# Optimization experiments

Measured on AMD Instinct MI355X. Metric: run time of the kernel, lower is better.

The kernel has to match this reference:

```python
import jax, jax.numpy as jnp
import numpy as np

HIDDEN = 1024
N_HEADS = 16
HEAD_DIM = HIDDEN // N_HEADS  # 64
B, N = 2, 2048
SCALE = HIDDEN ** (-0.5)  # NOTE: original scales by full hidden_size, not head_dim


def setup_inputs() -> dict:
    key = jax.random.key(0)
    k1, k2 = jax.random.split(key)
    hidden_states = jax.random.normal(k1, (B, N, HIDDEN), dtype=jnp.float32)
    attention_mask = jnp.ones((B, N), dtype=jnp.int32)
    # per-head no-bias Linear(hidden -> 3*head_dim), stacked: [h, hidden, 3*head_dim]
    W_qkv = jax.random.normal(k2, (N_HEADS, HIDDEN, 3 * HEAD_DIM), dtype=jnp.float32) * (HIDDEN ** -0.5)
    return {"hidden_states": hidden_states, "attention_mask": attention_mask, "W_qkv": W_qkv}


def reference(hidden_states, attention_mask, W_qkv):
    # qkv: [b, h, n, 3*d]
    qkv = jnp.einsum('bnD,hDe->bhne', hidden_states, W_qkv)
    q, k, v = jnp.split(qkv, 3, axis=-1)  # each [b, h, n, d]
    scores = jnp.einsum('bhid,bhjd->bhij', q, k) * SCALE
    mask = attention_mask[:, None, None, :] == 0  # [b,1,1,n]
    scores = jnp.where(mask, -jnp.inf, scores)
    attn = jax.nn.softmax(scores, axis=-1)
    out = jnp.einsum('bhij,bhjd->bhid', attn, v)  # [b, h, n, d]
    # rearrange 'b h n d -> b n (h d)'
    return jnp.transpose(out, (0, 2, 1, 3)).reshape(out.shape[0], out.shape[2], -1)
```

## Files before the change

kernel.cpp:

```cpp
#include <hip/hip_runtime.h>
#include <hip/hip_bf16.h>


#define NH   16
#define HD   64
#define SEQ  2048
#define HID  1024
#define E3   192
#define QSCALE 0.04508422017f
#define MBIAS  -43.2808512f

typedef __attribute__((ext_vector_type(8))) short short8;
typedef __attribute__((ext_vector_type(4))) float f32x4;
typedef __attribute__((ext_vector_type(16))) float f32x16;
typedef unsigned short ushort_t;

#define MFMA16(a, b, c) __builtin_amdgcn_mfma_f32_16x16x32_bf16((a), (b), (c), 0, 0, 0)
#define MFMA32(a, b, c) __builtin_amdgcn_mfma_f32_32x32x16_bf16((a), (b), (c), 0, 0, 0)

#if __has_builtin(__builtin_amdgcn_exp2f)
#define EXP2(x) __builtin_amdgcn_exp2f(x)
#else
#define EXP2(x) exp2f(x)
#endif

static __device__ __forceinline__ ushort_t f2bf(float x) {
    unsigned u = __builtin_bit_cast(unsigned, x);
    unsigned r = u + 0x7fff + ((u >> 16) & 1);
    return (ushort_t)(r >> 16);
}

static __device__ __forceinline__ unsigned pack_trunc(float hi, float lo) {
#if __has_builtin(__builtin_amdgcn_perm)
    return __builtin_amdgcn_perm(__builtin_bit_cast(unsigned, hi),
                                 __builtin_bit_cast(unsigned, lo), 0x07060302u);
#else
    return (__builtin_bit_cast(unsigned, hi) & 0xffff0000u) |
           (__builtin_bit_cast(unsigned, lo) >> 16);
#endif
}

static __device__ __forceinline__ void load_lds16(const void* g, void* l) {
    __builtin_amdgcn_global_load_lds(
        (__attribute__((address_space(1))) void*)(g),
        (__attribute__((address_space(3))) void*)(l), 16, 0, 0);
}

__global__ __launch_bounds__(256) void k_cvt_x(const void* __restrict__ Xv,
                                               ushort_t* __restrict__ Xb,
                                               int* __restrict__ flagp) {
    __shared__ int cnt;
    if (threadIdx.x == 0) cnt = 0;
    __syncthreads();
    const unsigned* X32 = (const unsigned*)Xv;
    if (threadIdx.x < 64) {
        unsigned u = X32[(size_t)blockIdx.x * 2048 + threadIdx.x * 32 + 7];
        int bexp = (u >> 7) & 0xFF;
        if (bexp >= 0x68 && bexp <= 0x90) atomicAdd(&cnt, 1);
    }
    __syncthreads();
    const int isf32 = (cnt < 32);
    if (blockIdx.x == 0 && threadIdx.x == 0) *flagp = isf32;

    const size_t base = ((size_t)blockIdx.x * 256 + threadIdx.x) * 16;
    if (isf32) {
        const float* Xf = (const float*)Xv;
        ushort_t tmp[16];
#pragma unroll
        for (int c = 0; c < 4; ++c) {
            float4 v = *(const float4*)(Xf + base + c * 4);
            tmp[c * 4 + 0] = f2bf(v.x); tmp[c * 4 + 1] = f2bf(v.y);
            tmp[c * 4 + 2] = f2bf(v.z); tmp[c * 4 + 3] = f2bf(v.w);
        }
        *(float4*)(Xb + base)     = ((const float4*)tmp)[0];
        *(float4*)(Xb + base + 8) = ((const float4*)tmp)[1];
    } else {
        const ushort_t* Xh = (const ushort_t*)Xv;
        *(float4*)(Xb + base)     = *(const float4*)(Xh + base);
        *(float4*)(Xb + base + 8) = *(const float4*)(Xh + base + 8);
    }
}

__global__ __launch_bounds__(256) void k_cvt_w(const void* __restrict__ Wv,
                                               ushort_t* __restrict__ Wt,
                                               const int* __restrict__ flagp) {
    __shared__ ushort_t tile[64][72];
    const int isf32 = *flagp;
    const int h  = blockIdx.x;
    const int dt = blockIdx.y;
    const int et = blockIdx.z;
    const int D0 = dt * 64, e0 = et * 64;
    const int t  = threadIdx.x;
#pragma unroll
    for (int r = 0; r < 2; ++r) {
        int row = r * 32 + (t >> 3);
        int col = (t & 7) * 8;
        size_t base = ((size_t)(h * HID + D0 + row)) * E3 + e0 + col;
        if (isf32) {
            const float* Wf = (const float*)Wv;
            float4 a = *(const float4*)(Wf + base);
            float4 c = *(const float4*)(Wf + base + 4);
            tile[row][col + 0] = f2bf(a.x); tile[row][col + 1] = f2bf(a.y);
            tile[row][col + 2] = f2bf(a.z); tile[row][col + 3] = f2bf(a.w);
            tile[row][col + 4] = f2bf(c.x); tile[row][col + 5] = f2bf(c.y);
            tile[row][col + 6] = f2bf(c.z); tile[row][col + 7] = f2bf(c.w);
        } else {
            *(float4*)&tile[row][col] = *(const float4*)((const ushort_t*)Wv + base);
        }
    }
    __syncthreads();
#pragma unroll
    for (int r = 0; r < 2; ++r) {
        int erow = r * 32 + (t >> 3);
        int dcol = (t & 7) * 8;
        ushort_t vals[8];
#pragma unroll
        for (int i = 0; i < 8; ++i) vals[i] = tile[dcol + i][erow];
        *(float4*)(Wt + ((size_t)(h * E3 + e0 + erow)) * HID + D0 + dcol) = *(float4*)vals;
    }
}

__global__ __launch_bounds__(256) void k_qkv(const ushort_t* __restrict__ Xb,
                                             const ushort_t* __restrict__ Wt,
                                             ushort_t* __restrict__ Qb,
                                             ushort_t* __restrict__ Kb,
                                             ushort_t* __restrict__ Vtb) {
    __shared__ __align__(16) ushort_t smem[2 * 128 * 64];
    ushort_t* Xl = smem;
    ushort_t* Wl = smem + 128 * 64;

    const int e0 = blockIdx.x * 128;
    const int m0 = blockIdx.y * 128;
    const int b  = m0 >> 11;
    const int n0 = m0 & 2047;
    const int t = threadIdx.x;
    const int w = t >> 6, lane = t & 63, l15 = lane & 15, quad = lane >> 4;
    const int wrow0 = (w & 1) * 64, wcol0 = (w >> 1) * 64;
    const int srow = lane >> 3;
    const int scb  = (lane & 7) ^ srow;

    f32x4 acc[4][4];
#pragma unroll
    for (int i = 0; i < 4; ++i)
#pragma unroll
        for (int j = 0; j < 4; ++j) acc[i][j] = (f32x4){0.f, 0.f, 0.f, 0.f};

    for (int k0 = 0; k0 < HID; k0 += 64) {
        __syncthreads();
#pragma unroll
        for (int cc = 0; cc < 4; ++cc) {
            const int ch  = w * 4 + cc;
            const int row = ch * 8 + srow;
            load_lds16(Xb + (size_t)(m0 + row) * HID + k0 + scb * 8, &Xl[ch * 512]);
            load_lds16(Wt + (size_t)(e0 + row) * HID + k0 + scb * 8, &Wl[ch * 512]);
        }
        __syncthreads();
#pragma unroll
        for (int kh = 0; kh < 2; ++kh) {
            short8 af[4], bfm[4];
#pragma unroll
            for (int i = 0; i < 4; ++i) {
                const int r = wrow0 + i * 16 + l15;
                af[i] = *(const short8*)&Xl[r * 64 + ((kh * 4 + quad) ^ (r & 7)) * 8];
            }
#pragma unroll
            for (int j = 0; j < 4; ++j) {
                const int r = wcol0 + j * 16 + l15;
                bfm[j] = *(const short8*)&Wl[r * 64 + ((kh * 4 + quad) ^ (r & 7)) * 8];
            }
#pragma unroll
            for (int i = 0; i < 4; ++i)
#pragma unroll
                for (int j = 0; j < 4; ++j)
                    acc[i][j] = MFMA16(af[i], bfm[j], acc[i][j]);
        }
    }

    __syncthreads();
#pragma unroll
    for (int p = 0; p < 2; ++p) {
        const int E0  = e0 + p * 64;
        const int hh  = E0 / 192;
        const int r0p = E0 - hh * 192;
        const int own = ((w >> 1) == p);
        if (r0p < 128) {
            if (own) {
                const float sc = (r0p == 0) ? QSCALE : 1.0f;
#pragma unroll
                for (int i = 0; i < 4; ++i)
#pragma unroll
                    for (int j = 0; j < 4; ++j)
#pragma unroll
                        for (int reg = 0; reg < 4; ++reg)
                            smem[(wrow0 + i * 16 + quad * 4 + reg) * 72 + j * 16 + l15] =
                                f2bf(acc[i][j][reg] * sc);
            }
            __syncthreads();
            ushort_t* dstb = (r0p == 0) ? Qb : Kb;
            const int r = t >> 1, part = t & 1;
            size_t dst = ((size_t)(b * NH + hh) * SEQ + n0 + r) * HD + part * 32;
#pragma unroll
            for (int c = 0; c < 4; ++c)
                *(float4*)(dstb + dst + c * 8) = *(const float4*)&smem[r * 72 + part * 32 + c * 8];
        } else {
            if (own) {
#pragma unroll
                for (int i = 0; i < 4; ++i)
#pragma unroll
                    for (int j = 0; j < 4; ++j)
#pragma unroll
                        for (int reg = 0; reg < 4; ++reg)
                            smem[(j * 16 + l15) * 136 + wrow0 + i * 16 + quad * 4 + reg] =
                                f2bf(acc[i][j][reg]);
            }
            __syncthreads();
            const int dr = t >> 2, part = t & 3;
            size_t dst = ((size_t)(b * NH + hh) * HD + dr) * SEQ + n0 + part * 32;
#pragma unroll
            for (int c = 0; c < 4; ++c)
                *(float4*)(Vtb + dst + c * 8) = *(const float4*)&smem[dr * 136 + part * 32 + c * 8];
        }
        if (p == 0) __syncthreads();
    }
}


#define SMPACK(sv, h0v, h1v)                                                  \
    {                                                                         \
        _Pragma("unroll")                                                     \
        for (int g = 0; g < 4; ++g) {                                         \
            float p0 = EXP2(sv[4*g+0]); float p1 = EXP2(sv[4*g+1]);           \
            float p2 = EXP2(sv[4*g+2]); float p3 = EXP2(sv[4*g+3]);           \
            l_r += (p0 + p1) + (p2 + p3);                                     \
            unsigned a0 = pack_trunc(p1, p0), a1 = pack_trunc(p3, p2);        \
            unsigned b0 = a0, b1 = a1;                                        \
            asm volatile("v_permlane32_swap_b32 %0, %1" : "+v"(a0), "+v"(b0));\
            asm volatile("v_permlane32_swap_b32 %0, %1" : "+v"(a1), "+v"(b1));\
            h0v[g*2+0] = a0; h1v[g*2+0] = b0;                                 \
            h0v[g*2+1] = a1; h1v[g*2+1] = b1;                                 \
        }                                                                     \
    }

#define MAKE_PB(dst, h0v, h1v, GB)                                            \
    {                                                                         \
        unsigned w0_ = hi ? h0v[(GB+1)*2+0] : h0v[(GB)*2+0];                  \
        unsigned w1_ = hi ? h0v[(GB+1)*2+1] : h0v[(GB)*2+1];                  \
        unsigned w2_ = hi ? h1v[(GB+1)*2+0] : h1v[(GB)*2+0];                  \
        unsigned w3_ = hi ? h1v[(GB+1)*2+1] : h1v[(GB)*2+1];                  \
        uint4 u_ = {w0_, w1_, w2_, w3_};                                      \
        dst = __builtin_bit_cast(short8, u_);                                 \
    }

__global__ __launch_bounds__(512, 4) void k_attn(const ushort_t* __restrict__ Qb,
                                                 const ushort_t* __restrict__ Kb,
                                                 const ushort_t* __restrict__ Vtb,
                                                 const int* __restrict__ mask,
                                                 void* __restrict__ outv,
                                                 const int* __restrict__ flagp) {
    __shared__ __align__(16) char smem_raw[73728];
    float* biasl = (float*)(smem_raw + 65536);

    const int isf32 = *flagp;
    const int q0 = blockIdx.x * 128;
    const int bh = blockIdx.y;
    const int b  = bh >> 4, h = bh & 15;
    const int t  = threadIdx.x;
    const int w  = t >> 6, lane = t & 63;
    const int wq = w >> 1, jh = w & 1;
    const int c31 = lane & 31, hi = lane >> 5;
    const int srow8 = lane >> 3;
    const int scb   = (lane & 7) ^ srow8;
    const int vrow4 = lane >> 4;
    const int vb15  = lane & 15;
    const int rx7   = c31 & 7;
    const int rx15  = c31 & 15;

    {
        ushort_t* kb = (ushort_t*)(smem_raw);
        ushort_t* vb = (ushort_t*)(smem_raw + 16384);
#pragma unroll
        for (int c = 0; c < 2; ++c) {
            const int krow = w * 16 + c * 8 + srow8;
            load_lds16(Kb + ((size_t)bh * SEQ + krow) * HD + scb * 8,
                       &kb[(w * 2 + c) * 512]);
            const int vrow = w * 8 + c * 4 + vrow4;
            load_lds16(Vtb + ((size_t)bh * HD + vrow) * SEQ + ((vb15 ^ (vrow & 15)) * 8),
                       &vb[(w * 2 + c) * 512]);
        }
    }

    int lm = 0;
    for (int i = t; i < SEQ; i += 512) {
        int mv = mask[b * SEQ + i];
        biasl[i] = mv ? 0.0f : MBIAS;
        lm |= (mv == 0);
    }
    const int qrow = q0 + wq * 32 + c31;
    short8 qB[4];
#pragma unroll
    for (int ds = 0; ds < 4; ++ds)
        qB[ds] = *(const short8*)(Qb + ((size_t)bh * SEQ + qrow) * HD + ds * 16 + hi * 8);

    const int use_bias = __syncthreads_or(lm);

    const f32x16 z16 = {0.f,0.f,0.f,0.f,0.f,0.f,0.f,0.f,0.f,0.f,0.f,0.f,0.f,0.f,0.f,0.f};
    f32x16 oa = z16, ob = z16;
    float l_r = 0.f;

    for (int j0 = 0; j0 < SEQ; j0 += 128) {
        const int idx = (j0 >> 7) & 1;
        asm volatile("s_waitcnt vmcnt(0)" ::: "memory");
        __builtin_amdgcn_s_barrier();
        asm volatile("" ::: "memory");
        if (j0 + 128 < SEQ) {
            ushort_t* kb2 = (ushort_t*)(smem_raw + (idx ^ 1) * 32768);
            ushort_t* vb2 = kb2 + 8192;
#pragma unroll
            for (int c = 0; c < 2; ++c) {
                const int krow = w * 16 + c * 8 + srow8;
                load_lds16(Kb + ((size_t)bh * SEQ + j0 + 128 + krow) * HD + scb * 8,
                           &kb2[(w * 2 + c) * 512]);
                const int vrow = w * 8 + c * 4 + vrow4;
                load_lds16(Vtb + ((size_t)bh * HD + vrow) * SEQ + j0 + 128 + ((vb15 ^ (vrow & 15)) * 8),
                           &vb2[(w * 2 + c) * 512]);
            }
        }
        ushort_t* kb = (ushort_t*)(smem_raw + idx * 32768);
        ushort_t* vb = kb + 8192;

        const int jr0 = jh * 64 + c31;
        const int jr1 = jh * 64 + 32 + c31;
        f32x16 s0, s1;
        __builtin_amdgcn_s_setprio(1);
#pragma unroll
        for (int ds = 0; ds < 4; ++ds) {
            short8 kf0 = *(const short8*)&kb[jr0 * 64 + (((2 * ds + hi) ^ rx7) * 8)];
            short8 kf1 = *(const short8*)&kb[jr1 * 64 + (((2 * ds + hi) ^ rx7) * 8)];
            s0 = MFMA32(kf0, qB[ds], ds ? s0 : z16);
            s1 = MFMA32(kf1, qB[ds], ds ? s1 : z16);
        }
        __builtin_amdgcn_s_setprio(0);
        if (use_bias) {
#pragma unroll
            for (int g = 0; g < 4; ++g) {
                float4 bj0 = *(const float4*)&biasl[j0 + jh * 64 + 8 * g + 4 * hi];
                float4 bj1 = *(const float4*)&biasl[j0 + jh * 64 + 32 + 8 * g + 4 * hi];
                s0[4*g+0] += bj0.x; s0[4*g+1] += bj0.y; s0[4*g+2] += bj0.z; s0[4*g+3] += bj0.w;
                s1[4*g+0] += bj1.x; s1[4*g+1] += bj1.y; s1[4*g+2] += bj1.z; s1[4*g+3] += bj1.w;
            }
        }

        unsigned h0a[8], h1a[8], h0b[8], h1b[8];
        SMPACK(s0, h0a, h1a);
        SMPACK(s1, h0b, h1b);

        __builtin_amdgcn_s_setprio(1);
#pragma unroll
        for (int half = 0; half < 2; ++half) {
#pragma unroll
            for (int c13 = 0; c13 < 2; ++c13) {
                short8 pb;
                if (half == 0) { MAKE_PB(pb, h0a, h1a, 2 * c13); }
                else           { MAKE_PB(pb, h0b, h1b, 2 * c13); }
                const int pblk = (jh * 4 + half * 2 + c13) * 2 + hi;
                short8 va0 = *(const short8*)&vb[(c31)      * 128 + ((pblk ^ rx15) * 8)];
                short8 va1 = *(const short8*)&vb[(32 + c31) * 128 + ((pblk ^ rx15) * 8)];
                oa = MFMA32(va0, pb, oa);
                ob = MFMA32(va1, pb, ob);
            }
        }
        __builtin_amdgcn_s_setprio(0);
    }

    float l_h = l_r + __shfl_xor(l_r, 32);

    __syncthreads();
    float* Obuf = (float*)smem_raw;
    float* Lbuf = (float*)(smem_raw + 65536);
    const int slot = (wq * 64 + lane) * 36;
    if (jh == 1) {
#pragma unroll
        for (int g = 0; g < 4; ++g) {
            *(float4*)&Obuf[slot + g * 4]      = (float4){oa[4*g], oa[4*g+1], oa[4*g+2], oa[4*g+3]};
            *(float4*)&Obuf[slot + 16 + g * 4] = (float4){ob[4*g], ob[4*g+1], ob[4*g+2], ob[4*g+3]};
        }
        Lbuf[wq * 64 + lane] = l_h;
    }
    __syncthreads();
    float rinv = 0.f;
    if (jh == 0) {
        const float l_tot = l_h + Lbuf[wq * 64 + lane];
        rinv = 1.0f / l_tot;
#pragma unroll
        for (int g = 0; g < 4; ++g) {
            float4 pa = *(const float4*)&Obuf[slot + g * 4];
            float4 pb4 = *(const float4*)&Obuf[slot + 16 + g * 4];
            oa[4*g] += pa.x; oa[4*g+1] += pa.y; oa[4*g+2] += pa.z; oa[4*g+3] += pa.w;
            ob[4*g] += pb4.x; ob[4*g+1] += pb4.y; ob[4*g+2] += pb4.z; ob[4*g+3] += pb4.w;
        }
    }
    __syncthreads();

    const int qlr = wq * 32 + c31;
    const int r = t >> 2, part = t & 3;
    if (!isf32) {
        ushort_t* Ol = (ushort_t*)smem_raw;
        if (jh == 0) {
#pragma unroll
            for (int dt = 0; dt < 2; ++dt) {
                const f32x16 ov = dt ? ob : oa;
#pragma unroll
                for (int g = 0; g < 4; ++g) {
                    const int d0 = dt * 32 + 8 * g + 4 * hi;
                    uint2 u;
                    u.x = (unsigned)f2bf(ov[4*g+0] * rinv) | ((unsigned)f2bf(ov[4*g+1] * rinv) << 16);
                    u.y = (unsigned)f2bf(ov[4*g+2] * rinv) | ((unsigned)f2bf(ov[4*g+3] * rinv) << 16);
                    *(uint2*)&Ol[qlr * 72 + d0] = u;
                }
            }
        }
        __syncthreads();
        ushort_t* outp = (ushort_t*)outv;
        size_t dst = ((size_t)b * SEQ + q0 + r) * HID + h * HD + part * 16;
        float4 v0 = *(const float4*)&Ol[r * 72 + part * 16];
        float4 v1 = *(const float4*)&Ol[r * 72 + part * 16 + 8];
        *(float4*)(outp + dst)     = v0;
        *(float4*)(outp + dst + 8) = v1;
    } else {
        float* Olf = (float*)smem_raw;
        if (jh == 0) {
#pragma unroll
            for (int dt = 0; dt < 2; ++dt) {
                const f32x16 ov = dt ? ob : oa;
#pragma unroll
                for (int g = 0; g < 4; ++g) {
                    const int d0 = dt * 32 + 8 * g + 4 * hi;
                    float4 fv;
                    fv.x = ov[4*g+0] * rinv; fv.y = ov[4*g+1] * rinv;
                    fv.z = ov[4*g+2] * rinv; fv.w = ov[4*g+3] * rinv;
                    *(float4*)&Olf[qlr * 68 + d0] = fv;
                }
            }
        }
        __syncthreads();
        float* outp = (float*)outv;
        size_t dst = ((size_t)b * SEQ + q0 + r) * HID + h * HD + part * 16;
#pragma unroll
        for (int c = 0; c < 4; ++c) {
            float4 v = *(const float4*)&Olf[r * 68 + part * 16 + c * 4];
            *(float4*)(outp + dst + c * 4) = v;
        }
    }
}

extern "C" void kernel_launch(void* const* d_in, const int* in_sizes, int n_in,
                              void* d_out, int out_size, void* d_ws, size_t ws_size,
                              hipStream_t stream) {
    const void* X    = d_in[0];
    const int*  mask = (const int*)d_in[1];
    const void* W    = d_in[2];

    char* ws = (char*)d_ws;
    ushort_t* Qb    = (ushort_t*)(ws);
    ushort_t* Kb    = (ushort_t*)(ws + 8388608);
    ushort_t* Vtb   = (ushort_t*)(ws + 16777216);
    ushort_t* Wtb   = (ushort_t*)(ws + 25165824);
    int*      flagp = (int*)(ws + 31457280);
    ushort_t* Xb    = (ushort_t*)d_out;

    k_cvt_x<<<1024, 256, 0, stream>>>(X, Xb, flagp);
    k_cvt_w<<<dim3(16, 16, 3), 256, 0, stream>>>(W, Wtb, flagp);
    k_qkv<<<dim3(24, 32), 256, 0, stream>>>(Xb, Wtb, Qb, Kb, Vtb);
    k_attn<<<dim3(16, 32), 512, 0, stream>>>(Qb, Kb, Vtb, mask, d_out, flagp);
}
```

Measured before the change: 178.1 us.

## Merge X/W conversion kernels and remap block IDs for XCD-local L2 reuse

Fuses the X and W bf16 conversion kernels into one launch. The W blocks now detect fp32 versus bf16 on their own instead of reading the flag written by the X kernel, which removes one launch and the dependency between the two. It also remaps block indices in the QKV GEMM and attention kernels so that consecutive blocks on the same XCD share weight columns or the same (batch, head) K/V. The goal is better L2 locality on the MI355X's partitioned caches. Each W block now runs its own dtype heuristic on W data, which could disagree with the X-based flag.

```diff
diff --git a/kernel.cpp b/kernel.cpp
--- a/kernel.cpp
+++ b/kernel.cpp
@@ -46,77 +46,87 @@
         (__attribute__((address_space(3))) void*)(l), 16, 0, 0);
 }
 
-__global__ __launch_bounds__(256) void k_cvt_x(const void* __restrict__ Xv,
-                                               ushort_t* __restrict__ Xb,
-                                               int* __restrict__ flagp) {
+__global__ __launch_bounds__(256) void k_cvt(const void* __restrict__ Xv,
+                                             const void* __restrict__ Wv,
+                                             ushort_t* __restrict__ Xb,
+                                             ushort_t* __restrict__ Wt,
+                                             int* __restrict__ flagp) {
     __shared__ int cnt;
+    __shared__ ushort_t tile[64][72];
+    const int t = threadIdx.x;
     if (threadIdx.x == 0) cnt = 0;
     __syncthreads();
-    const unsigned* X32 = (const unsigned*)Xv;
-    if (threadIdx.x < 64) {
-        unsigned u = X32[(size_t)blockIdx.x * 2048 + threadIdx.x * 32 + 7];
-        int bexp = (u >> 7) & 0xFF;
-        if (bexp >= 0x68 && bexp <= 0x90) atomicAdd(&cnt, 1);
-    }
-    __syncthreads();
-    const int isf32 = (cnt < 32);
-    if (blockIdx.x == 0 && threadIdx.x == 0) *flagp = isf32;
-
-    const size_t base = ((size_t)blockIdx.x * 256 + threadIdx.x) * 16;
-    if (isf32) {
-        const float* Xf = (const float*)Xv;
-        ushort_t tmp[16];
-#pragma unroll
-        for (int c = 0; c < 4; ++c) {
-            float4 v = *(const float4*)(Xf + base + c * 4);
-            tmp[c * 4 + 0] = f2bf(v.x); tmp[c * 4 + 1] = f2bf(v.y);
-            tmp[c * 4 + 2] = f2bf(v.z); tmp[c * 4 + 3] = f2bf(v.w);
-        }
-        *(float4*)(Xb + base)     = ((const float4*)tmp)[0];
-        *(float4*)(Xb + base + 8) = ((const float4*)tmp)[1];
+
+    if (blockIdx.x < 1024) {
+        const unsigned* X32 = (const unsigned*)Xv;
+        if (t < 64) {
+            unsigned u = X32[(size_t)blockIdx.x * 2048 + t * 32 + 7];
+            int bexp = (u >> 7) & 0xFF;
+            if (bexp >= 0x68 && bexp <= 0x90) atomicAdd(&cnt, 1);
+        }
+        __syncthreads();
+        const int isf32 = (cnt < 32);
+        if (blockIdx.x == 0 && t == 0) *flagp = isf32;
+
+        const size_t base = ((size_t)blockIdx.x * 256 + t) * 16;
+        if (isf32) {
+            const float* Xf = (const float*)Xv;
+            ushort_t tmp[16];
+#pragma unroll
+            for (int c = 0; c < 4; ++c) {
+                float4 v = *(const float4*)(Xf + base + c * 4);
+                tmp[c * 4 + 0] = f2bf(v.x); tmp[c * 4 + 1] = f2bf(v.y);
+                tmp[c * 4 + 2] = f2bf(v.z); tmp[c * 4 + 3] = f2bf(v.w);
+            }
+            *(float4*)(Xb + base)     = ((const float4*)tmp)[0];
+            *(float4*)(Xb + base + 8) = ((const float4*)tmp)[1];
+        } else {
+            const ushort_t* Xh = (const ushort_t*)Xv;
+            *(float4*)(Xb + base)     = *(const float4*)(Xh + base);
+            *(float4*)(Xb + base + 8) = *(const float4*)(Xh + base + 8);
+        }
     } else {
-        const ushort_t* Xh = (const ushort_t*)Xv;
-        *(float4*)(Xb + base)     = *(const float4*)(Xh + base);
-        *(float4*)(Xb + base + 8) = *(const float4*)(Xh + base + 8);
-    }
-}
-
-__global__ __launch_bounds__(256) void k_cvt_w(const void* __restrict__ Wv,
-                                               ushort_t* __restrict__ Wt,
-                                               const int* __restrict__ flagp) {
-    __shared__ ushort_t tile[64][72];
-    const int isf32 = *flagp;
-    const int h  = blockIdx.x;
-    const int dt = blockIdx.y;
-    const int et = blockIdx.z;
-    const int D0 = dt * 64, e0 = et * 64;
-    const int t  = threadIdx.x;
-#pragma unroll
-    for (int r = 0; r < 2; ++r) {
-        int row = r * 32 + (t >> 3);
-        int col = (t & 7) * 8;
-        size_t base = ((size_t)(h * HID + D0 + row)) * E3 + e0 + col;
-        if (isf32) {
-            const float* Wf = (const float*)Wv;
-            float4 a = *(const float4*)(Wf + base);
-            float4 c = *(const float4*)(Wf + base + 4);
-            tile[row][col + 0] = f2bf(a.x); tile[row][col + 1] = f2bf(a.y);
-            tile[row][col + 2] = f2bf(a.z); tile[row][col + 3] = f2bf(a.w);
-            tile[row][col + 4] = f2bf(c.x); tile[row][col + 5] = f2bf(c.y);
-            tile[row][col + 6] = f2bf(c.z); tile[row][col + 7] = f2bf(c.w);
-        } else {
-            *(float4*)&tile[row][col] = *(const float4*)((const ushort_t*)Wv + base);
-        }
-    }
-    __syncthreads();
-#pragma unroll
-    for (int r = 0; r < 2; ++r) {
-        int erow = r * 32 + (t >> 3);
-        int dcol = (t & 7) * 8;
-        ushort_t vals[8];
-#pragma unroll
-        for (int i = 0; i < 8; ++i) vals[i] = tile[dcol + i][erow];
-        *(float4*)(Wt + ((size_t)(h * E3 + e0 + erow)) * HID + D0 + dcol) = *(float4*)vals;
+        const int wb = blockIdx.x - 1024;
+        const unsigned* W32 = (const unsigned*)Wv;
+        if (t < 64) {
+            unsigned u = W32[(size_t)wb * 2048 + t * 32 + 7];
+            int bexp = (u >> 7) & 0xFF;
+            if (bexp >= 0x68 && bexp <= 0x90) atomicAdd(&cnt, 1);
+        }
+        __syncthreads();
+        const int isf32 = (cnt < 32);
+
+        const int h  = wb & 15;
+        const int dt = (wb >> 4) & 15;
+        const int et = wb >> 8;
+        const int D0 = dt * 64, e0 = et * 64;
+#pragma unroll
+        for (int r = 0; r < 2; ++r) {
+            int row = r * 32 + (t >> 3);
+            int col = (t & 7) * 8;
+            size_t base = ((size_t)(h * HID + D0 + row)) * E3 + e0 + col;
+            if (isf32) {
+                const float* Wf = (const float*)Wv;
+                float4 a = *(const float4*)(Wf + base);
+                float4 c = *(const float4*)(Wf + base + 4);
+                tile[row][col + 0] = f2bf(a.x); tile[row][col + 1] = f2bf(a.y);
+                tile[row][col + 2] = f2bf(a.z); tile[row][col + 3] = f2bf(a.w);
+                tile[row][col + 4] = f2bf(c.x); tile[row][col + 5] = f2bf(c.y);
+                tile[row][col + 6] = f2bf(c.z); tile[row][col + 7] = f2bf(c.w);
+            } else {
+                *(float4*)&tile[row][col] = *(const float4*)((const ushort_t*)Wv + base);
+            }
+        }
+        __syncthreads();
+#pragma unroll
+        for (int r = 0; r < 2; ++r) {
+            int erow = r * 32 + (t >> 3);
+            int dcol = (t & 7) * 8;
+            ushort_t vals[8];
+#pragma unroll
+            for (int i = 0; i < 8; ++i) vals[i] = tile[dcol + i][erow];
+            *(float4*)(Wt + ((size_t)(h * E3 + e0 + erow)) * HID + D0 + dcol) = *(float4*)vals;
+        }
     }
 }
 
@@ -129,8 +139,10 @@
     ushort_t* Xl = smem;
     ushort_t* Wl = smem + 128 * 64;
 
-    const int e0 = blockIdx.x * 128;
-    const int m0 = blockIdx.y * 128;
+    const int bid = blockIdx.y * 24 + blockIdx.x;
+    const int xcd = bid & 7, pos = bid >> 3;
+    const int e0 = (xcd * 3 + (pos >> 5)) * 128;
+    const int m0 = (pos & 31) * 128;
     const int b  = m0 >> 11;
     const int n0 = m0 & 2047;
     const int t = threadIdx.x;
@@ -261,8 +273,10 @@
     float* biasl = (float*)(smem_raw + 65536);
 
     const int isf32 = *flagp;
-    const int q0 = blockIdx.x * 128;
-    const int bh = blockIdx.y;
+    const int bidl = blockIdx.y * 16 + blockIdx.x;
+    const int xcd8 = bidl & 7, posx = bidl >> 3;
+    const int bh   = xcd8 * 4 + (posx >> 4);
+    const int q0   = (posx & 15) * 128;
     const int b  = bh >> 4, h = bh & 15;
     const int t  = threadIdx.x;
     const int w  = t >> 6, lane = t & 63;
@@ -468,8 +482,7 @@
     int*      flagp = (int*)(ws + 31457280);
     ushort_t* Xb    = (ushort_t*)d_out;
 
-    k_cvt_x<<<1024, 256, 0, stream>>>(X, Xb, flagp);
-    k_cvt_w<<<dim3(16, 16, 3), 256, 0, stream>>>(W, Wtb, flagp);
+    k_cvt<<<1792, 256, 0, stream>>>(X, W, Xb, Wtb, flagp);
     k_qkv<<<dim3(24, 32), 256, 0, stream>>>(Xb, Wtb, Qb, Kb, Vtb);
     k_attn<<<dim3(16, 32), 512, 0, stream>>>(Qb, Kb, Vtb, mask, d_out, flagp);
 }
```

After: 179.0 us. No clear change (+0.5%).
